# Kernel optimization log

Hardware: AMD Instinct MI355X
Metric: run time of the kernel (lower is better)

## Reference

```python
import jax, jax.numpy as jnp
import numpy as np

NUM_HEADS = 8
DIMS = 512
SR = 2
EPS = 1e-6


def setup_inputs() -> dict:
    key = jax.random.key(0)
    ks = jax.random.split(key, 12)
    B, H, W, C = 4, 64, 64, DIMS
    s = 0.02
    return {
        "x": jax.random.normal(ks[0], (B, H * W, C), dtype=jnp.float32),
        "Wq": jax.random.normal(ks[1], (C, DIMS), dtype=jnp.float32) * s,
        "bq": jnp.zeros((DIMS,), jnp.float32),
        "Wk": jax.random.normal(ks[2], (C, DIMS), dtype=jnp.float32) * s,
        "bk": jnp.zeros((DIMS,), jnp.float32),
        "Wv": jax.random.normal(ks[3], (C, DIMS), dtype=jnp.float32) * s,
        "bv": jnp.zeros((DIMS,), jnp.float32),
        "Wp": jax.random.normal(ks[4], (DIMS, DIMS), dtype=jnp.float32) * s,
        "bp": jnp.zeros((DIMS,), jnp.float32),
        "sr_w": jax.random.normal(ks[5], (SR, SR, C, DIMS), dtype=jnp.float32) * s,  # HWIO
        "sr_b": jnp.zeros((DIMS,), jnp.float32),
        "ln_g": jnp.ones((DIMS,), jnp.float32),
        "ln_b": jnp.zeros((DIMS,), jnp.float32),
        "H": 64,
        "W": 64,
    }


def reference(x, Wq, bq, Wk, bk, Wv, bv, Wp, bp, sr_w, sr_b, ln_g, ln_b, H, W):
    B, N, C = x.shape
    hd = DIMS // NUM_HEADS

    # spatial-reduction of K/V: strided conv (kernel=stride=SR, SAME) + LayerNorm
    kv = x.reshape(B, H, W, C)
    kv = jax.lax.conv_general_dilated(
        kv, sr_w, window_strides=(SR, SR), padding="SAME",
        dimension_numbers=("NHWC", "HWIO", "NHWC")) + sr_b
    kv = kv.reshape(B, -1, C)  # [B, Nk, C], Nk = (H//SR)*(W//SR)
    mu = jnp.mean(kv, axis=-1, keepdims=True)
    var = jnp.mean(jnp.square(kv - mu), axis=-1, keepdims=True)
    kv = (kv - mu) * jax.lax.rsqrt(var + EPS) * ln_g + ln_b
    Nk = kv.shape[1]

    # NOTE: original splits heads as reshape(B, N, head_dims, num_heads) and
    # indexes the LAST axis per head -> head h sees channels d*NUM_HEADS+h.
    q = (x @ Wq + bq).reshape(B, N, hd, NUM_HEADS)
    k = (kv @ Wk + bk).reshape(B, Nk, hd, NUM_HEADS)
    v = (kv @ Wv + bv).reshape(B, Nk, hd, NUM_HEADS)

    scores = jnp.einsum("bqdh,bkdh->bhqk", q, k) / jnp.sqrt(jnp.float32(hd))
    w = jax.nn.softmax(scores, axis=-1)
    # concat of heads along channels -> (B, N, NUM_HEADS, hd) layout
    out = jnp.einsum("bhqk,bkdh->bqhd", w, v).reshape(B, N, DIMS)
    return out @ Wp + bp
```

## Files before the change

kernel.cpp:

```cpp
#include <hip/hip_runtime.h>


typedef __attribute__((ext_vector_type(8))) _Float16 f16x8;
typedef __attribute__((ext_vector_type(4))) _Float16 f16x4;
typedef __attribute__((ext_vector_type(4))) float f32x4;

#define EXP2F(x) __builtin_amdgcn_exp2f(x)

__device__ __forceinline__ void gload_lds16(const _Float16* g, _Float16* l)
{
    __builtin_amdgcn_global_load_lds(
        (const __attribute__((address_space(1))) void*)g,
        (__attribute__((address_space(3))) void*)l, 16, 0, 0);
}

__global__ __launch_bounds__(256)
void prep_k(const float* __restrict__ x,
            const float* __restrict__ Wq, const float* __restrict__ Wk,
            const float* __restrict__ Wv, const float* __restrict__ Wp,
            const float* __restrict__ srw,
            _Float16* __restrict__ xh, _Float16* __restrict__ wqt,
            _Float16* __restrict__ wkvt, _Float16* __restrict__ wpt,
            _Float16* __restrict__ srwt)
{
    __shared__ float T[32][33];
    const int id = blockIdx.x;
    const int t = threadIdx.x;

    if (id < 4096) {
        const size_t i = ((size_t)id * 256 + t) * 8;
        const float4 a = *(const float4*)(x + i);
        const float4 b = *(const float4*)(x + i + 4);
        f16x8 o;
        o[0] = (_Float16)a.x; o[1] = (_Float16)a.y; o[2] = (_Float16)a.z; o[3] = (_Float16)a.w;
        o[4] = (_Float16)b.x; o[5] = (_Float16)b.y; o[6] = (_Float16)b.z; o[7] = (_Float16)b.w;
        *(f16x8*)(xh + i) = o;
        return;
    }

    if (id < 5120) {
        const int id2 = id - 4096;
        const int z = id2 >> 8, k0 = ((id2 >> 4) & 15) * 32, n0 = (id2 & 15) * 32;
        const float* src; _Float16* dst; int perm;
        switch (z) {
            case 0:  src = Wq; dst = wqt;           perm = 1; break;
            case 1:  src = Wk; dst = wkvt;          perm = 1; break;
            case 2:  src = Wv; dst = wkvt + 262144; perm = 0; break;
            default: src = Wp; dst = wpt;           perm = 0; break;
        }
        {
            const int r = t >> 3, c = (t & 7) * 4;
            const float4 v = *(const float4*)(src + (size_t)(k0 + r) * 512 + n0 + c);
            T[r][c + 0] = v.x; T[r][c + 1] = v.y; T[r][c + 2] = v.z; T[r][c + 3] = v.w;
        }
        __syncthreads();
        {
            const int j = t >> 3, i0 = (t & 7) * 4;
            const int n = n0 + j;
            const int nper = perm ? ((n & 7) * 64 + (n >> 3)) : n;
            f16x4 o;
            o[0] = (_Float16)T[i0 + 0][j];
            o[1] = (_Float16)T[i0 + 1][j];
            o[2] = (_Float16)T[i0 + 2][j];
            o[3] = (_Float16)T[i0 + 3][j];
            *(f16x4*)(dst + (size_t)nper * 512 + k0 + i0) = o;
        }
        return;
    }

    {
        const int id3 = id - 5120;
        const int n0 = (id3 & 15) * 32, k0 = (id3 >> 4) * 32;
        {
            const int r = t >> 3, c = (t & 7) * 4;
            const float4 v = *(const float4*)(srw + (size_t)(k0 + r) * 512 + n0 + c);
            T[r][c + 0] = v.x; T[r][c + 1] = v.y; T[r][c + 2] = v.z; T[r][c + 3] = v.w;
        }
        __syncthreads();
        {
            const int j = t >> 3, i0 = (t & 7) * 4;
            f16x4 o;
            o[0] = (_Float16)T[i0 + 0][j];
            o[1] = (_Float16)T[i0 + 1][j];
            o[2] = (_Float16)T[i0 + 2][j];
            o[3] = (_Float16)T[i0 + 3][j];
            *(f16x4*)(srwt + (size_t)(n0 + j) * 2048 + k0 + i0) = o;
        }
        return;
    }
}

template<int MODE, bool CONV, int BM>
__device__ __forceinline__ void gemm_body(
    const int bx, const int by,
    const _Float16* __restrict__ A, const _Float16* __restrict__ Wt,
    const float* __restrict__ bias, const float* __restrict__ bias2,
    void* __restrict__ Cv, void* __restrict__ Cv2,
    _Float16* __restrict__ As, _Float16* __restrict__ Ws)
{
    constexpr int K = CONV ? 2048 : 512;
    constexpr int MT = BM / 32;
    constexpr int AI = BM / 64;
    const int tid = threadIdx.x;
    const int wave = tid >> 6, lane = tid & 63;
    const int quad = lane >> 4, l15 = lane & 15;
    const int wm = wave >> 1, wn = wave & 1;
    const int wrow = wm * (BM / 2);
    const int m0 = by * BM, n0 = bx * 128;

    f32x4 acc[MT][4] = {};

    for (int k0 = 0; k0 < K; k0 += 32) {
        __syncthreads();
        #pragma unroll
        for (int t = 0; t < AI; ++t) {
            const int ii = wave * AI + t;
            const int e = ii * 64 + lane;
            const int row = e >> 2, c8 = (e & 3) * 8;
            const _Float16* gp;
            if (CONV) {
                const int grow = m0 + row;
                const int b = grow >> 10, rem = grow & 1023;
                const int oh = rem >> 5, ow = rem & 31;
                const int gk = k0 + c8;
                const int ky = (gk >> 10) & 1, kx = (gk >> 9) & 1, ci = gk & 511;
                gp = A + ((size_t)((b * 64 + 2 * oh + ky) * 64) + (2 * ow + kx)) * 512 + ci;
            } else {
                gp = A + (size_t)(m0 + row) * K + k0 + c8;
            }
            gload_lds16(gp, &As[ii * 512]);
        }
        #pragma unroll
        for (int t = 0; t < 2; ++t) {
            const int ii = wave * 2 + t;
            const int e = ii * 64 + lane;
            const int row = e >> 2, c8 = (e & 3) * 8;
            gload_lds16(Wt + (size_t)(n0 + row) * K + k0 + c8, &Ws[ii * 512]);
        }
        __syncthreads();

        f16x8 af[MT], bf[4];
        #pragma unroll
        for (int mt = 0; mt < MT; ++mt)
            af[mt] = *(const f16x8*)&As[(wrow + mt * 16 + l15) * 32 + quad * 8];
        #pragma unroll
        for (int nt = 0; nt < 4; ++nt)
            bf[nt] = *(const f16x8*)&Ws[(wn * 64 + nt * 16 + l15) * 32 + quad * 8];
        #pragma unroll
        for (int mt = 0; mt < MT; ++mt)
            #pragma unroll
            for (int nt = 0; nt < 4; ++nt)
                acc[mt][nt] = __builtin_amdgcn_mfma_f32_16x16x32_f16(
                    af[mt], bf[nt], acc[mt][nt], 0, 0, 0);
    }

    #pragma unroll
    for (int nt = 0; nt < 4; ++nt) {
        const int gcol = n0 + wn * 64 + nt * 16 + l15;
        float bv;
        if (MODE == 6) bv = bias[(gcol & 63) * 8 + (gcol >> 6)];
        else if (MODE == 5) bv = (gcol < 512) ? bias[(gcol & 63) * 8 + (gcol >> 6)]
                                              : bias2[gcol - 512];
        else bv = bias[gcol];
        #pragma unroll
        for (int mt = 0; mt < MT; ++mt) {
            const int row0 = m0 + wrow + mt * 16 + quad * 4;
            if (MODE == 0) {
                #pragma unroll
                for (int r = 0; r < 4; ++r)
                    ((float*)Cv)[(size_t)(row0 + r) * 512 + gcol] = acc[mt][nt][r] + bv;
            } else if (MODE == 4 || MODE == 6) {
                #pragma unroll
                for (int r = 0; r < 4; ++r)
                    ((_Float16*)Cv)[(size_t)(row0 + r) * 512 + gcol] =
                        (_Float16)(acc[mt][nt][r] + bv);
            } else {
                if (gcol < 512) {
                    #pragma unroll
                    for (int r = 0; r < 4; ++r)
                        ((_Float16*)Cv)[(size_t)(row0 + r) * 512 + gcol] =
                            (_Float16)(acc[mt][nt][r] + bv);
                } else {
                    const int c = gcol - 512;
                    const int h = c & 7, d = c >> 3;
                    const int b_ = row0 >> 10, jj = row0 & 1023;
                    f16x4 o;
                    #pragma unroll
                    for (int r = 0; r < 4; ++r) o[r] = (_Float16)(acc[mt][nt][r] + bv);
                    *(f16x4*)((_Float16*)Cv2 +
                              ((size_t)(b_ * 8 + h) * 64 + d) * 1024 + jj) = o;
                }
            }
        }
    }
}

template<int MODE, bool CONV, int BM>
__global__ __launch_bounds__(256)
void gemm_f16(const _Float16* __restrict__ A, const _Float16* __restrict__ Wt,
              const float* __restrict__ bias, const float* __restrict__ bias2,
              void* __restrict__ Cv, void* __restrict__ Cv2)
{
    __shared__ __align__(16) _Float16 As[BM * 32];
    __shared__ __align__(16) _Float16 Ws[128 * 32];
    gemm_body<MODE, CONV, BM>(blockIdx.x, blockIdx.y, A, Wt, bias, bias2,
                              Cv, Cv2, As, Ws);
}

__global__ __launch_bounds__(256)
void convq_k(const _Float16* __restrict__ xh, const _Float16* __restrict__ srwt,
             const float* __restrict__ srb, const _Float16* __restrict__ wqt,
             const float* __restrict__ bq,
             _Float16* __restrict__ kvh, _Float16* __restrict__ qh)
{
    __shared__ __align__(16) _Float16 As[128 * 32];
    __shared__ __align__(16) _Float16 Ws[128 * 32];
    const int id = blockIdx.x;
    if (id < 512) {
        gemm_body<6, false, 128>(id & 3, id >> 2, xh, wqt, bq, nullptr,
                                 qh, nullptr, As, Ws);
    } else {
        const int id2 = id - 512;
        gemm_body<4, true, 64>(id2 & 3, id2 >> 2, xh, srwt, srb, nullptr,
                               kvh, nullptr, As, Ws);
    }
}

__global__ __launch_bounds__(256)
void ln_k(_Float16* __restrict__ buf, const float* __restrict__ g,
          const float* __restrict__ b)
{
    const int row = blockIdx.x;
    _Float16* p = buf + (size_t)row * 512;
    const int tid = threadIdx.x;
    const float vx = (float)p[tid * 2], vy = (float)p[tid * 2 + 1];
    float s = vx + vy, q = vx * vx + vy * vy;
    #pragma unroll
    for (int off = 32; off > 0; off >>= 1) {
        s += __shfl_xor(s, off);
        q += __shfl_xor(q, off);
    }
    __shared__ float ss[4], sq[4], stat[2];
    const int wid = tid >> 6;
    if ((tid & 63) == 0) { ss[wid] = s; sq[wid] = q; }
    __syncthreads();
    if (tid == 0) {
        const float S = ss[0] + ss[1] + ss[2] + ss[3];
        const float Q = sq[0] + sq[1] + sq[2] + sq[3];
        const float mu = S * (1.f / 512.f);
        const float var = fmaxf(Q * (1.f / 512.f) - mu * mu, 0.f);
        stat[0] = mu;
        stat[1] = rsqrtf(var + 1e-6f);
    }
    __syncthreads();
    const float mu = stat[0], rs = stat[1];
    const float2 gg = *(const float2*)(g + tid * 2);
    const float2 bb = *(const float2*)(b + tid * 2);
    p[tid * 2]     = (_Float16)((vx - mu) * rs * gg.x + bb.x);
    p[tid * 2 + 1] = (_Float16)((vy - mu) * rs * gg.y + bb.y);
}

__global__ __launch_bounds__(512)
void attn_mfma_k(const _Float16* __restrict__ qb,
                 const _Float16* __restrict__ kbuf,
                 const _Float16* __restrict__ vbuf,
                 _Float16* __restrict__ out)
{
    const int bh = blockIdx.y;
    const int qt = blockIdx.x;
    const int b = bh >> 3, h = bh & 7;
    const int tid = threadIdx.x;
    const int wave = tid >> 6, lane = tid & 63;
    const int quad = lane >> 4, l15 = lane & 15;

    __shared__ __align__(16) _Float16 Ks[2][64 * 72];
    __shared__ __align__(16) _Float16 Vs[2][64 * 72];

    const int qrow = b * 4096 + qt * 512 + wave * 64 + l15;
    const _Float16* qp = qb + (size_t)qrow * 512 + h * 64 + quad * 8;
    f16x8 qf[4][2];
    #pragma unroll
    for (int su = 0; su < 4; ++su) {
        qf[su][0] = *(const f16x8*)(qp + su * 16 * 512);
        qf[su][1] = *(const f16x8*)(qp + su * 16 * 512 + 32);
    }
    {
        const _Float16 qs = (_Float16)0.18033688f;
        #pragma unroll
        for (int su = 0; su < 4; ++su)
            #pragma unroll
            for (int g = 0; g < 2; ++g)
                #pragma unroll
                for (int i = 0; i < 8; ++i) qf[su][g][i] *= qs;
    }

    const int kr = tid >> 3, kc = (tid & 7) * 8;
    const int krp = (kr & 32) | ((kr & 4) << 2) | ((kr >> 1) & 12) | (kr & 3);
    const _Float16* kg = kbuf + (size_t)(b * 1024 + kr) * 512 + h * 64 + kc;
    const _Float16* vg = vbuf + (size_t)(bh * 64 + kr) * 1024 + kc;

    f16x8 krg = *(const f16x8*)kg;
    f16x8 vrg = *(const f16x8*)vg;
    *(f16x8*)&Ks[0][krp * 72 + kc] = krg;
    *(f16x8*)&Vs[0][kr * 72 + kc] = vrg;

    float l_run[4] = {0.f, 0.f, 0.f, 0.f};
    f32x4 acc[4][4] = {};

    for (int kt = 0; kt < 16; ++kt) {
        const int cur = kt & 1;
        __syncthreads();
        if (kt < 15) {
            krg = *(const f16x8*)(kg + (size_t)(kt + 1) * 64 * 512);
            vrg = *(const f16x8*)(vg + (kt + 1) * 64);
        }

        #pragma unroll
        for (int kb = 0; kb < 2; ++kb) {
            f16x8 pa[4];
            #pragma unroll
            for (int c = 0; c < 2; ++c) {
                const int ct = kb * 2 + c;
                const f16x8 kf0 = *(const f16x8*)&Ks[cur][(ct * 16 + l15) * 72 + quad * 8];
                const f16x8 kf1 = *(const f16x8*)&Ks[cur][(ct * 16 + l15) * 72 + 32 + quad * 8];
                #pragma unroll
                for (int su = 0; su < 4; ++su) {
                    f32x4 s = {};
                    s = __builtin_amdgcn_mfma_f32_16x16x32_f16(kf0, qf[su][0], s, 0, 0, 0);
                    s = __builtin_amdgcn_mfma_f32_16x16x32_f16(kf1, qf[su][1], s, 0, 0, 0);
                    const float p0 = EXP2F(s[0]), p1 = EXP2F(s[1]);
                    const float p2 = EXP2F(s[2]), p3 = EXP2F(s[3]);
                    l_run[su] += (p0 + p1) + (p2 + p3);
                    pa[su][c * 4 + 0] = (_Float16)p0;
                    pa[su][c * 4 + 1] = (_Float16)p1;
                    pa[su][c * 4 + 2] = (_Float16)p2;
                    pa[su][c * 4 + 3] = (_Float16)p3;
                }
            }
            __builtin_amdgcn_s_setprio(1);
            #pragma unroll
            for (int nt = 0; nt < 4; ++nt) {
                const f16x8 vf = *(const f16x8*)&Vs[cur][(nt * 16 + l15) * 72 + kb * 32 + quad * 8];
                #pragma unroll
                for (int su = 0; su < 4; ++su)
                    acc[su][nt] = __builtin_amdgcn_mfma_f32_16x16x32_f16(
                        pa[su], vf, acc[su][nt], 0, 0, 0);
            }
            __builtin_amdgcn_s_setprio(0);
        }

        if (kt < 15) {
            *(f16x8*)&Ks[cur ^ 1][krp * 72 + kc] = krg;
            *(f16x8*)&Vs[cur ^ 1][kr * 72 + kc] = vrg;
        }
    }

    #pragma unroll
    for (int su = 0; su < 4; ++su) {
        float ts = l_run[su];
        ts += __shfl_xor(ts, 16);
        ts += __shfl_xor(ts, 32);
        float inv[4];
        #pragma unroll
        for (int r = 0; r < 4; ++r)
            inv[r] = 1.0f / __shfl(ts, quad * 4 + r, 16);
        #pragma unroll
        for (int nt = 0; nt < 4; ++nt)
            #pragma unroll
            for (int r = 0; r < 4; ++r) {
                const int row = qt * 512 + wave * 64 + su * 16 + quad * 4 + r;
                const int col = h * 64 + nt * 16 + l15;
                out[((size_t)b * 4096 + row) * 512 + col] =
                    (_Float16)(acc[su][nt][r] * inv[r]);
            }
    }
}

extern "C" void kernel_launch(void* const* d_in, const int* in_sizes, int n_in,
                              void* d_out, int out_size, void* d_ws, size_t ws_size,
                              hipStream_t stream)
{
    const float* x   = (const float*)d_in[0];
    const float* Wq  = (const float*)d_in[1];
    const float* bq  = (const float*)d_in[2];
    const float* Wk  = (const float*)d_in[3];
    const float* bk  = (const float*)d_in[4];
    const float* Wv  = (const float*)d_in[5];
    const float* bv  = (const float*)d_in[6];
    const float* Wp  = (const float*)d_in[7];
    const float* bp  = (const float*)d_in[8];
    const float* srw = (const float*)d_in[9];
    const float* srb = (const float*)d_in[10];
    const float* lng = (const float*)d_in[11];
    const float* lnb = (const float*)d_in[12];

    _Float16* ws   = (_Float16*)d_ws;
    _Float16* xh   = ws;
    _Float16* atth = xh + 8388608;
    _Float16* kvh  = atth + 8388608;
    _Float16* kh   = kvh + 2097152;
    _Float16* vh   = kh + 2097152;
    _Float16* wqt  = vh + 2097152;
    _Float16* wkvt = wqt + 262144;
    _Float16* wpt  = wkvt + 524288;
    _Float16* srwt = wpt + 262144;
    _Float16* qh   = (_Float16*)d_out;

    prep_k<<<6144, 256, 0, stream>>>(x, Wq, Wk, Wv, Wp, srw,
                                     xh, wqt, wkvt, wpt, srwt);
    convq_k<<<768, 256, 0, stream>>>(xh, srwt, srb, wqt, bq, kvh, qh);
    ln_k<<<4096, 256, 0, stream>>>(kvh, lng, lnb);
    gemm_f16<5, false, 64><<<dim3(8, 64), 256, 0, stream>>>(
        kvh, wkvt, bk, bv, kh, vh);
    attn_mfma_k<<<dim3(8, 32), 512, 0, stream>>>(qh, kh, vh, atth);
    gemm_f16<0, false, 128><<<dim3(4, 128), 256, 0, stream>>>(
        atth, wpt, bp, nullptr, d_out, nullptr);
}
```

Before: 223.4 us.

## Double-buffer GEMM LDS tiles and schedule conv blocks before Q blocks

The shared GEMM body now uses two LDS buffers for the A and W tiles. It issues the global-to-LDS loads for the next K slice before running the MFMAs on the current one, and needs one barrier per iteration instead of two. The fused conv+Q kernel also reorders its block IDs so the longer K=2048 conv blocks launch first, which should improve tail balance. The cost is double the LDS footprint, which may reduce occupancy.

```diff
diff --git a/kernel.cpp b/kernel.cpp
--- a/kernel.cpp
+++ b/kernel.cpp
@@ -99,8 +99,10 @@
     _Float16* __restrict__ As, _Float16* __restrict__ Ws)
 {
     constexpr int K = CONV ? 2048 : 512;
+    constexpr int NIT = K / 32;
     constexpr int MT = BM / 32;
     constexpr int AI = BM / 64;
+    constexpr int ABUF = BM * 32;
     const int tid = threadIdx.x;
     const int wave = tid >> 6, lane = tid & 63;
     const int quad = lane >> 4, l15 = lane & 15;
@@ -110,8 +112,7 @@
 
     f32x4 acc[MT][4] = {};
 
-    for (int k0 = 0; k0 < K; k0 += 32) {
-        __syncthreads();
+    auto stage = [&](const int k0, const int buf) {
         #pragma unroll
         for (int t = 0; t < AI; ++t) {
             const int ii = wave * AI + t;
@@ -128,30 +129,42 @@
             } else {
                 gp = A + (size_t)(m0 + row) * K + k0 + c8;
             }
-            gload_lds16(gp, &As[ii * 512]);
+            gload_lds16(gp, &As[buf * ABUF + ii * 512]);
         }
         #pragma unroll
         for (int t = 0; t < 2; ++t) {
             const int ii = wave * 2 + t;
             const int e = ii * 64 + lane;
             const int row = e >> 2, c8 = (e & 3) * 8;
-            gload_lds16(Wt + (size_t)(n0 + row) * K + k0 + c8, &Ws[ii * 512]);
-        }
-        __syncthreads();
+            gload_lds16(Wt + (size_t)(n0 + row) * K + k0 + c8,
+                        &Ws[buf * 4096 + ii * 512]);
+        }
+    };
+
+    stage(0, 0);
+    asm volatile("s_waitcnt vmcnt(0)" ::: "memory");
+    __builtin_amdgcn_s_barrier();
+
+    for (int it = 0; it < NIT; ++it) {
+        const int cur = it & 1;
+        if (it + 1 < NIT) stage((it + 1) * 32, cur ^ 1);
 
         f16x8 af[MT], bf[4];
         #pragma unroll
         for (int mt = 0; mt < MT; ++mt)
-            af[mt] = *(const f16x8*)&As[(wrow + mt * 16 + l15) * 32 + quad * 8];
+            af[mt] = *(const f16x8*)&As[cur * ABUF + (wrow + mt * 16 + l15) * 32 + quad * 8];
         #pragma unroll
         for (int nt = 0; nt < 4; ++nt)
-            bf[nt] = *(const f16x8*)&Ws[(wn * 64 + nt * 16 + l15) * 32 + quad * 8];
+            bf[nt] = *(const f16x8*)&Ws[cur * 4096 + (wn * 64 + nt * 16 + l15) * 32 + quad * 8];
         #pragma unroll
         for (int mt = 0; mt < MT; ++mt)
             #pragma unroll
             for (int nt = 0; nt < 4; ++nt)
                 acc[mt][nt] = __builtin_amdgcn_mfma_f32_16x16x32_f16(
                     af[mt], bf[nt], acc[mt][nt], 0, 0, 0);
+
+        asm volatile("s_waitcnt vmcnt(0)" ::: "memory");
+        __builtin_amdgcn_s_barrier();
     }
 
     #pragma unroll
@@ -201,8 +214,8 @@
               const float* __restrict__ bias, const float* __restrict__ bias2,
               void* __restrict__ Cv, void* __restrict__ Cv2)
 {
-    __shared__ __align__(16) _Float16 As[BM * 32];
-    __shared__ __align__(16) _Float16 Ws[128 * 32];
+    __shared__ __align__(16) _Float16 As[2 * BM * 32];
+    __shared__ __align__(16) _Float16 Ws[2 * 128 * 32];
     gemm_body<MODE, CONV, BM>(blockIdx.x, blockIdx.y, A, Wt, bias, bias2,
                               Cv, Cv2, As, Ws);
 }
@@ -213,16 +226,16 @@
              const float* __restrict__ bq,
              _Float16* __restrict__ kvh, _Float16* __restrict__ qh)
 {
-    __shared__ __align__(16) _Float16 As[128 * 32];
-    __shared__ __align__(16) _Float16 Ws[128 * 32];
+    __shared__ __align__(16) _Float16 As[2 * 128 * 32];
+    __shared__ __align__(16) _Float16 Ws[2 * 128 * 32];
     const int id = blockIdx.x;
-    if (id < 512) {
-        gemm_body<6, false, 128>(id & 3, id >> 2, xh, wqt, bq, nullptr,
+    if (id < 256) {
+        gemm_body<4, true, 64>(id & 3, id >> 2, xh, srwt, srb, nullptr,
+                               kvh, nullptr, As, Ws);
+    } else {
+        const int id2 = id - 256;
+        gemm_body<6, false, 128>(id2 & 3, id2 >> 2, xh, wqt, bq, nullptr,
                                  qh, nullptr, As, Ws);
-    } else {
-        const int id2 = id - 512;
-        gemm_body<4, true, 64>(id2 & 3, id2 >> 2, xh, srwt, srb, nullptr,
-                               kvh, nullptr, As, Ws);
     }
 }
 
```

After: 227.9 us. 1.02x slower.
